# Kernel optimization log

Measured on AMD Instinct MI355X. Metric: run time of the kernel, lower is better.

## Reference

```python
import jax, jax.numpy as jnp
import numpy as np

EMBED_DIM = 1024
NUM_HEADS = 16
N_POS = 2048
BATCH = 4


def setup_inputs() -> dict:
    key = jax.random.key(0)
    k_x, k_w1, k_b1, k_wo, k_bo = jax.random.split(key, 5)
    s1 = 1.0 / np.sqrt(EMBED_DIM)
    x = jax.random.normal(k_x, (BATCH, N_POS, EMBED_DIM), dtype=jnp.float32)
    # torch Linear weights stored as [in, out] for x @ W + b
    W_qkv = jax.random.uniform(k_w1, (EMBED_DIM, 3 * EMBED_DIM), dtype=jnp.float32, minval=-s1, maxval=s1)
    b_qkv = jax.random.uniform(k_b1, (3 * EMBED_DIM,), dtype=jnp.float32, minval=-s1, maxval=s1)
    W_o = jax.random.uniform(k_wo, (EMBED_DIM, EMBED_DIM), dtype=jnp.float32, minval=-s1, maxval=s1)
    b_o = jax.random.uniform(k_bo, (EMBED_DIM,), dtype=jnp.float32, minval=-s1, maxval=s1)
    return {"x": x, "W_qkv": W_qkv, "b_qkv": b_qkv, "W_o": W_o, "b_o": b_o}


def reference(x, W_qkv, b_qkv, W_o, b_o):
    B, N, C = x.shape
    H = NUM_HEADS
    d_k = C // H
    qkv = x @ W_qkv + b_qkv                       # [B, N, 3C]
    q, k, v = jnp.split(qkv, 3, axis=-1)
    q = q.reshape(B, N, H, d_k).transpose(0, 2, 1, 3)  # [B, H, N, d_k]
    k = k.reshape(B, N, H, d_k).transpose(0, 2, 1, 3)
    v = v.reshape(B, N, H, d_k).transpose(0, 2, 1, 3)
    scores = jnp.einsum('bhqd,bhkd->bhqk', q, k) * (1.0 / np.sqrt(d_k))
    causal = jnp.tril(jnp.ones((N, N), dtype=bool))
    scores = jnp.where(causal, scores, -jnp.inf)
    attn = jax.nn.softmax(scores, axis=-1)
    out = jnp.einsum('bhqk,bhkd->bhqd', attn, v)  # [B, H, N, d_k]
    out = out.transpose(0, 2, 1, 3).reshape(B, N, C)
    return out @ W_o + b_o
```

## Files before the change

### kernel.cpp

```cpp
#include <hip/hip_runtime.h>
#include <hip/hip_bf16.h>

typedef __attribute__((ext_vector_type(8))) __bf16 bf16x8;
typedef __attribute__((ext_vector_type(4))) float f32x4;
typedef __attribute__((ext_vector_type(16))) float f32x16;
typedef __attribute__((ext_vector_type(4))) unsigned short u16x4;
typedef __attribute__((ext_vector_type(8))) unsigned short u16x8;
typedef __attribute__((ext_vector_type(4))) unsigned int u32x4;
typedef unsigned short u16;

#define MFMA16 __builtin_amdgcn_mfma_f32_16x16x32_bf16
#define MFMA32 __builtin_amdgcn_mfma_f32_32x32x16_bf16

#if __has_builtin(__builtin_amdgcn_exp2f)
#define EXP2F __builtin_amdgcn_exp2f
#else
#define EXP2F(x) __expf((x) * 0.69314718056f)
#endif

__device__ inline u16 f32_to_bf16_bits(float f) {
    unsigned u = __builtin_bit_cast(unsigned, f);
    unsigned r = u + 0x7FFFu + ((u >> 16) & 1u);
    return (u16)(r >> 16);
}

__device__ inline void g2l16(const void* g, void* l) {
    __builtin_amdgcn_global_load_lds(
        (const __attribute__((address_space(1))) unsigned int*)g,
        (__attribute__((address_space(3))) unsigned int*)l,
        16, 0, 0);
}

__device__ inline float red32_max(float x) { return fmaxf(x, __shfl_xor(x, 32)); }
__device__ inline float red32_sum(float x) { return x + __shfl_xor(x, 32); }

__global__ void cvt_bf16_kernel(const float* __restrict__ in, u16* __restrict__ out, int n) {
    int i = (blockIdx.x * 256 + threadIdx.x) * 4;
    if (i >= n) return;
    f32x4 v = *(const f32x4*)&in[i];
    u16x4 r;
#pragma unroll
    for (int j = 0; j < 4; ++j) r[j] = f32_to_bf16_bits(v[j]);
    *(u16x4*)&out[i] = r;
}

__global__ __launch_bounds__(256) void cvt_t_kernel(const float* __restrict__ W,
                                                    u16* __restrict__ WT, int K, int N) {
    const int w = threadIdx.x >> 6, l = threadIdx.x & 63;
    const int n = blockIdx.x * 64 + l;
    const int k0 = blockIdx.y * 32 + w * 8;
    u16x8 r;
#pragma unroll
    for (int i = 0; i < 8; ++i)
        r[i] = f32_to_bf16_bits(W[(size_t)(k0 + i) * N + n]);
    *(u16x8*)&WT[(size_t)n * K + k0] = r;
}

template <int STORE_BF16>
__global__ __launch_bounds__(256) void gemm_nt(
    const u16* __restrict__ A, const u16* __restrict__ BT,
    const float* __restrict__ bias, void* __restrict__ Cv,
    int M, int N, int K, int qcols, float qscale, int nbx)
{
    __shared__ __align__(16) u16 SM[24576];
    const int tid = threadIdx.x;
    const int w = tid >> 6, l = tid & 63;
    const int lr = l & 15, lh = l >> 4;
    const int wr = (w >> 1) * 64, wc = (w & 1) * 64;

    const int nwg = gridDim.x;
    const int swz = (blockIdx.x & 7) * (nwg >> 3) + (blockIdx.x >> 3);
    const int m0 = (swz / nbx) * 128;
    const int n0 = (swz % nbx) * 128;

    const int NT = K >> 5;

    const int f0 = tid, f1 = 256 + tid;
    const int r0 = f0 >> 2, r1 = f1 >> 2;
    const int cs0 = ((f0 & 3) ^ ((r0 >> 1) & 3)) * 8;
    const int cs1 = ((f1 & 3) ^ ((r1 >> 1) & 3)) * 8;
    const size_t arow0 = (size_t)(m0 + r0) * K, arow1 = (size_t)(m0 + r1) * K;
    const size_t brow0 = (size_t)(n0 + r0) * K, brow1 = (size_t)(n0 + r1) * K;

#define STAGE_TILE(t, set)                                                     \
    do {                                                                       \
        const int kk_ = (t) * 32;                                              \
        u16* dst_ = SM + (set) * 8192 + w * 512;                               \
        g2l16(A + arow0 + kk_ + cs0, dst_);                                    \
        g2l16(BT + brow0 + kk_ + cs0, dst_ + 4096);                            \
        g2l16(A + arow1 + kk_ + cs1, dst_ + 2048);                             \
        g2l16(BT + brow1 + kk_ + cs1, dst_ + 4096 + 2048);                     \
    } while (0)

    f32x4 acc[4][4];
#pragma unroll
    for (int m = 0; m < 4; ++m)
#pragma unroll
        for (int n = 0; n < 4; ++n) acc[m][n] = (f32x4)(0.0f);

    STAGE_TILE(0, 0);
    STAGE_TILE(1, 1);
    asm volatile("s_waitcnt vmcnt(4) lgkmcnt(0)\n\ts_barrier" ::: "memory");

    const int csw = (lr >> 1) & 3;
    int s0 = 0, s2 = 2;
    for (int t = 0; t < NT; ++t) {
        if (t + 2 < NT) STAGE_TILE(t + 2, s2);

        const u16* As = SM + s0 * 8192;
        const u16* Bs = As + 4096;
        bf16x8 af[4], bfr[4];
#pragma unroll
        for (int m = 0; m < 4; ++m)
            af[m] = *(const bf16x8*)&As[(wr + m * 16 + lr) * 32 + ((lh ^ csw) << 3)];
#pragma unroll
        for (int n = 0; n < 4; ++n)
            bfr[n] = *(const bf16x8*)&Bs[(wc + n * 16 + lr) * 32 + ((lh ^ csw) << 3)];
        __builtin_amdgcn_s_setprio(1);
#pragma unroll
        for (int m = 0; m < 4; ++m)
#pragma unroll
            for (int n = 0; n < 4; ++n)
                acc[m][n] = MFMA16(af[m], bfr[n], acc[m][n], 0, 0, 0);
        __builtin_amdgcn_s_setprio(0);

        if (t + 2 < NT)
            asm volatile("s_waitcnt vmcnt(4) lgkmcnt(0)\n\ts_barrier" ::: "memory");
        else if (t + 1 < NT)
            asm volatile("s_waitcnt vmcnt(0) lgkmcnt(0)\n\ts_barrier" ::: "memory");

        s0 = (s0 == 2) ? 0 : s0 + 1;
        s2 = (s2 == 2) ? 0 : s2 + 1;
    }
#undef STAGE_TILE

#pragma unroll
    for (int m = 0; m < 4; ++m) {
        int row = m0 + wr + m * 16 + lh * 4;
#pragma unroll
        for (int n = 0; n < 4; ++n) {
            int col = n0 + wc + n * 16 + lr;
            float bs = bias[col];
            float sc = (col < qcols) ? qscale : 1.0f;
#pragma unroll
            for (int j = 0; j < 4; ++j) {
                float v = (acc[m][n][j] + bs) * sc;
                if (STORE_BF16)
                    ((u16*)Cv)[(size_t)(row + j) * N + col] = f32_to_bf16_bits(v);
                else
                    ((float*)Cv)[(size_t)(row + j) * N + col] = v;
            }
        }
    }
}

__global__ __launch_bounds__(512, 1) void attn_kernel(
    const u16* __restrict__ qkv, u16* __restrict__ ctx)
{
    __shared__ __align__(16) u16 SM[32768];

    const int bid = blockIdx.x;
    const int xcd = bid & 7, jj = bid >> 3;
    const int bh = xcd * 8 + (jj >> 2);
    const int pr = jj & 3;
    const int b = bh >> 4, h = bh & 15;
    const size_t rowbase = (size_t)b * 2048;
    const int tid = threadIdx.x, w = tid >> 6, l = tid & 63;
    const int lq = l & 31, lk = l >> 5;

    const int rsub = l >> 3;
    const int cstage = l & 7;
    const int kchunk = cstage ^ rsub;

    bf16x8 vreg[2];

#pragma unroll
    for (int pass = 0; pass < 2; ++pass) {
        const int qt = pass ? (7 - pr) : pr;
        const int q0 = qt * 256;
        const int nt = 2 * qt + 2;
        const int qbase = q0 + w * 32;

        const u16* qp = qkv + (rowbase + qbase + lq) * 3072 + h * 64 + lk * 8;
        bf16x8 qf[4];
#pragma unroll
        for (int j = 0; j < 4; ++j) qf[j] = *(const bf16x8*)(qp + j * 16);

        f32x16 ot[2];
#pragma unroll
        for (int dt = 0; dt < 2; ++dt) ot[dt] = (f32x16)(0.0f);
        float m_run = -3e38f, l_run = 0.0f;

        __syncthreads();
#pragma unroll
        for (int p = 0; p < 2; ++p) {
            const int r = w * 16 + p * 8 + rsub;
            g2l16(qkv + (rowbase + r) * 3072 + 1024 + h * 64 + kchunk * 8,
                  SM + w * 1024 + p * 512);
            vreg[p] = *(const bf16x8*)(qkv + (rowbase + r) * 3072 + 2048 + h * 64 + cstage * 8);
        }
        asm volatile("s_waitcnt vmcnt(0)" ::: "memory");
#pragma unroll
        for (int p = 0; p < 2; ++p) {
            const int r = w * 16 + p * 8 + rsub;
#pragma unroll
            for (int i = 0; i < 8; ++i) {
                const int d = cstage * 8 + i;
                SM[16384 + ((d * 128 + r) ^ (((i ^ cstage) & 7) << 3))] = ((const u16*)&vreg[p])[i];
            }
        }
        __syncthreads();

        for (int t = 0; t < nt; ++t) {
            const int c = t & 1;
            const int kb = t * 128;
            u16* const Kb = SM + (c ? 8192 : 0);
            u16* const Vb = SM + 16384 + (c ? 8192 : 0);

            if (t + 1 < nt) {
                const int kb2 = kb + 128;
#pragma unroll
                for (int p = 0; p < 2; ++p) {
                    const int r = w * 16 + p * 8 + rsub;
                    g2l16(qkv + (rowbase + kb2 + r) * 3072 + 1024 + h * 64 + kchunk * 8,
                          SM + (c ? 0 : 8192) + w * 1024 + p * 512);
                    vreg[p] = *(const bf16x8*)(qkv + (rowbase + kb2 + r) * 3072 + 2048 + h * 64 + cstage * 8);
                }
            }

            if (kb <= qbase + 31) {
                bf16x8 kf[4][4];
#pragma unroll
                for (int kt = 0; kt < 4; ++kt)
#pragma unroll
                    for (int j = 0; j < 4; ++j)
                        kf[kt][j] = *(const bf16x8*)&Kb[((kt * 32 + lq) * 64 + j * 16 + lk * 8) ^ ((lq & 7) << 3)];

                f32x16 sf[4];
                __builtin_amdgcn_s_setprio(1);
#pragma unroll
                for (int kt = 0; kt < 4; ++kt) {
                    f32x16 z = (f32x16)(0.0f);
#pragma unroll
                    for (int j = 0; j < 4; ++j) z = MFMA32(kf[kt][j], qf[j], z, 0, 0, 0);
                    sf[kt] = z;
                }
                __builtin_amdgcn_s_setprio(0);

                float mt = -3e38f;
                if (kb + 127 > qbase) {
                    const int qrow = qbase + lq;
#pragma unroll
                    for (int kt = 0; kt < 4; ++kt)
#pragma unroll
                        for (int r = 0; r < 16; ++r) {
                            const int key = kb + kt * 32 + (r & 3) + 8 * (r >> 2) + 4 * lk;
                            float v = sf[kt][r];
                            if (key > qrow) v = -3e38f;
                            sf[kt][r] = v;
                            mt = fmaxf(mt, v);
                        }
                } else {
#pragma unroll
                    for (int kt = 0; kt < 4; ++kt)
#pragma unroll
                        for (int r = 0; r < 16; ++r) mt = fmaxf(mt, sf[kt][r]);
                }
                mt = red32_max(mt);

                const bool defer = __all(mt <= m_run + 16.0f);
                float mn = m_run;
                if (!defer) {
                    mn = fmaxf(m_run, mt);
                    const float alpha = EXP2F(m_run - mn);
                    m_run = mn;
                    l_run *= alpha;
#pragma unroll
                    for (int dt = 0; dt < 2; ++dt)
#pragma unroll
                        for (int r = 0; r < 16; ++r) ot[dt][r] *= alpha;
                }
                float rs = 0.0f;
#pragma unroll
                for (int kt = 0; kt < 4; ++kt)
#pragma unroll
                    for (int r = 0; r < 16; ++r) {
                        const float pp = EXP2F(sf[kt][r] - mn);
                        sf[kt][r] = pp;
                        rs += pp;
                    }
                l_run += red32_sum(rs);

                unsigned pc[4][4][2];
#pragma unroll
                for (int kt = 0; kt < 4; ++kt)
#pragma unroll
                    for (int rg = 0; rg < 4; ++rg) {
                        unsigned d0, d1;
                        asm("v_cvt_pk_bf16_f32 %0, %1, %2"
                            : "=v"(d0) : "v"((float)sf[kt][rg * 4 + 0]), "v"((float)sf[kt][rg * 4 + 1]));
                        asm("v_cvt_pk_bf16_f32 %0, %1, %2"
                            : "=v"(d1) : "v"((float)sf[kt][rg * 4 + 2]), "v"((float)sf[kt][rg * 4 + 3]));
                        pc[kt][rg][0] = d0;
                        pc[kt][rg][1] = d1;
                    }

                __builtin_amdgcn_s_setprio(1);
#pragma unroll
                for (int kt = 0; kt < 4; ++kt)
#pragma unroll
                    for (int hh = 0; hh < 2; ++hh) {
                        unsigned a0 = pc[kt][2 * hh][0], a1 = pc[kt][2 * hh][1];
                        unsigned b0 = pc[kt][2 * hh + 1][0], b1 = pc[kt][2 * hh + 1][1];
                        asm("v_permlane32_swap_b32 %0, %1" : "+v"(a0), "+v"(b0));
                        asm("v_permlane32_swap_b32 %0, %1" : "+v"(a1), "+v"(b1));
                        u32x4 wv = {a0, a1, b0, b1};
                        const bf16x8 pb = __builtin_bit_cast(bf16x8, wv);
                        const int k0 = 2 * kt + hh;
#pragma unroll
                        for (int dt = 0; dt < 2; ++dt) {
                            const int d = dt * 32 + lq;
                            const int vswz = ((d & 7) ^ (d >> 3)) & 7;
                            const bf16x8 vf = *(const bf16x8*)&Vb[((d * 128) + (k0 * 16 + lk * 8)) ^ (vswz << 3)];
                            ot[dt] = MFMA32(vf, pb, ot[dt], 0, 0, 0);
                        }
                    }
                __builtin_amdgcn_s_setprio(0);
            }

            asm volatile("s_waitcnt vmcnt(0)" ::: "memory");
            if (t + 1 < nt) {
                u16* const Vn = SM + 16384 + (c ? 0 : 8192);
#pragma unroll
                for (int p = 0; p < 2; ++p) {
                    const int r = w * 16 + p * 8 + rsub;
#pragma unroll
                    for (int i = 0; i < 8; ++i) {
                        const int d = cstage * 8 + i;
                        Vn[((d * 128 + r) ^ (((i ^ cstage) & 7) << 3))] = ((const u16*)&vreg[p])[i];
                    }
                }
            }
            __syncthreads();
        }

        u16* const out_l = SM + w * 2176;
        const float inv = 1.0f / l_run;
#pragma unroll
        for (int dt = 0; dt < 2; ++dt)
#pragma unroll
            for (int r = 0; r < 16; ++r) {
                const int d = dt * 32 + (r & 3) + 8 * (r >> 2) + 4 * lk;
                out_l[lq * 68 + d] = f32_to_bf16_bits(ot[dt][r] * inv);
            }
#pragma unroll
        for (int rr = 0; rr < 4; ++rr) {
            const int row = rr * 8 + (l >> 3);
            const bf16x8 v = *(const bf16x8*)&out_l[row * 68 + (l & 7) * 8];
            *(bf16x8*)(ctx + (rowbase + qbase + row) * 1024 + h * 64 + (l & 7) * 8) = v;
        }
    }
}

extern "C" void kernel_launch(void* const* d_in, const int* in_sizes, int n_in,
                              void* d_out, int out_size, void* d_ws, size_t ws_size,
                              hipStream_t stream) {
    const float* x      = (const float*)d_in[0];
    const float* W_qkv  = (const float*)d_in[1];
    const float* b_qkv  = (const float*)d_in[2];
    const float* W_o    = (const float*)d_in[3];
    const float* b_o    = (const float*)d_in[4];
    float* out = (float*)d_out;

    const int M = 4 * 2048;
    const int C = 1024;
    u16* qkv   = (u16*)d_ws;
    u16* xb    = qkv   + (size_t)M * 3 * C;
    u16* wqkvt = xb    + (size_t)M * C;
    u16* ctx   = wqkvt + (size_t)3 * C * C;
    u16* wot   = ctx   + (size_t)M * C;

    const float SCQ = 0.125f * 1.44269504089f;

    cvt_bf16_kernel<<<(M * C) / (256 * 4), 256, 0, stream>>>(x, xb, M * C);
    cvt_t_kernel<<<dim3(3 * C / 64, C / 32), 256, 0, stream>>>(W_qkv, wqkvt, C, 3 * C);
    cvt_t_kernel<<<dim3(C / 64, C / 32), 256, 0, stream>>>(W_o, wot, C, C);

    gemm_nt<1><<<(3 * C / 128) * (M / 128), 256, 0, stream>>>(xb, wqkvt, b_qkv, qkv,
                                                              M, 3 * C, C, C, SCQ, 3 * C / 128);

    attn_kernel<<<256, 512, 0, stream>>>(qkv, ctx);

    gemm_nt<0><<<(C / 128) * (M / 128), 256, 0, stream>>>(ctx, wot, b_o, out,
                                                          M, C, C, 0, 1.0f, C / 128);
}
```

Baseline: 167.0 us.

## Use 256x128 tile GEMM with triple-buffered LDS for QKV projection

Adds a new GEMM kernel for the QKV projection that computes 256x128 output tiles per workgroup, with each wave owning a 128x64 block. K-slices are held in a three-stage LDS ring buffer, and loads for step t+2 are issued while step t is being multiplied. The larger tile raises arithmetic intensity and the deeper pipeline is meant to hide global-load latency. The cost is more LDS and accumulator registers per workgroup, which may lower occupancy, and the grid is halved to 768 workgroups.

```diff
diff --git a/kernel.cpp b/kernel.cpp
--- a/kernel.cpp
+++ b/kernel.cpp
@@ -54,6 +54,109 @@
     for (int i = 0; i < 8; ++i)
         r[i] = f32_to_bf16_bits(W[(size_t)(k0 + i) * N + n]);
     *(u16x8*)&WT[(size_t)n * K + k0] = r;
+}
+
+template <int STORE_BF16>
+__global__ __launch_bounds__(256) void gemm_nt5(
+    const u16* __restrict__ A, const u16* __restrict__ BT,
+    const float* __restrict__ bias, void* __restrict__ Cv,
+    int M, int N, int K, int qcols, float qscale, int nbx)
+{
+    __shared__ __align__(16) u16 SM[36864];
+    const int tid = threadIdx.x;
+    const int w = tid >> 6, l = tid & 63;
+    const int lr = l & 15, lh = l >> 4;
+    const int wr = (w >> 1) * 128;
+    const int wc = (w & 1) * 64;
+
+    const int nwg = gridDim.x;
+    const int swz = (blockIdx.x & 7) * (nwg >> 3) + (blockIdx.x >> 3);
+    const int m0 = (swz / nbx) * 256;
+    const int n0 = (swz % nbx) * 128;
+
+    const int NT = K >> 5;
+
+    const int rr = tid >> 2;
+    const int cs = ((tid & 3) ^ ((tid >> 3) & 3)) * 8;
+    size_t aoff[4], boff[2];
+#pragma unroll
+    for (int p = 0; p < 4; ++p) aoff[p] = (size_t)(m0 + p * 64 + rr) * K + cs;
+#pragma unroll
+    for (int p = 0; p < 2; ++p) boff[p] = (size_t)(n0 + p * 64 + rr) * K + cs;
+    u16* const wbase = SM + (size_t)(tid >> 6) * 512;
+
+#define STAGE5(t, set)                                                         \
+    do {                                                                       \
+        const int kk_ = (t) * 32;                                              \
+        u16* d_ = wbase + (set) * 12288;                                       \
+        g2l16(A + aoff[0] + kk_, d_);                                          \
+        g2l16(A + aoff[1] + kk_, d_ + 2048);                                   \
+        g2l16(A + aoff[2] + kk_, d_ + 4096);                                   \
+        g2l16(A + aoff[3] + kk_, d_ + 6144);                                   \
+        g2l16(BT + boff[0] + kk_, d_ + 8192);                                  \
+        g2l16(BT + boff[1] + kk_, d_ + 10240);                                 \
+    } while (0)
+
+    f32x4 acc[8][4];
+#pragma unroll
+    for (int m = 0; m < 8; ++m)
+#pragma unroll
+        for (int n = 0; n < 4; ++n) acc[m][n] = (f32x4)(0.0f);
+
+    STAGE5(0, 0);
+    STAGE5(1, 1);
+    asm volatile("s_waitcnt vmcnt(6) lgkmcnt(0)\n\ts_barrier" ::: "memory");
+
+    const int csw = (lr >> 1) & 3;
+    int s0 = 0, s2 = 2;
+    for (int t = 0; t < NT; ++t) {
+        if (t + 2 < NT) STAGE5(t + 2, s2);
+
+        const u16* As = SM + s0 * 12288;
+        const u16* Bs = As + 8192;
+        bf16x8 af[8], bfr[4];
+#pragma unroll
+        for (int m = 0; m < 8; ++m)
+            af[m] = *(const bf16x8*)&As[(wr + m * 16 + lr) * 32 + ((lh ^ csw) << 3)];
+#pragma unroll
+        for (int n = 0; n < 4; ++n)
+            bfr[n] = *(const bf16x8*)&Bs[(wc + n * 16 + lr) * 32 + ((lh ^ csw) << 3)];
+        __builtin_amdgcn_s_setprio(1);
+#pragma unroll
+        for (int m = 0; m < 8; ++m)
+#pragma unroll
+            for (int n = 0; n < 4; ++n)
+                acc[m][n] = MFMA16(af[m], bfr[n], acc[m][n], 0, 0, 0);
+        __builtin_amdgcn_s_setprio(0);
+
+        if (t + 2 < NT)
+            asm volatile("s_waitcnt vmcnt(6) lgkmcnt(0)\n\ts_barrier" ::: "memory");
+        else if (t + 1 < NT)
+            asm volatile("s_waitcnt vmcnt(0) lgkmcnt(0)\n\ts_barrier" ::: "memory");
+
+        s0 = (s0 == 2) ? 0 : s0 + 1;
+        s2 = (s2 == 2) ? 0 : s2 + 1;
+    }
+#undef STAGE5
+
+#pragma unroll
+    for (int m = 0; m < 8; ++m) {
+        int row = m0 + wr + m * 16 + lh * 4;
+#pragma unroll
+        for (int n = 0; n < 4; ++n) {
+            int col = n0 + wc + n * 16 + lr;
+            float bs = bias[col];
+            float sc = (col < qcols) ? qscale : 1.0f;
+#pragma unroll
+            for (int j = 0; j < 4; ++j) {
+                float v = (acc[m][n][j] + bs) * sc;
+                if (STORE_BF16)
+                    ((u16*)Cv)[(size_t)(row + j) * N + col] = f32_to_bf16_bits(v);
+                else
+                    ((float*)Cv)[(size_t)(row + j) * N + col] = v;
+            }
+        }
+    }
 }
 
 template <int STORE_BF16>
@@ -386,8 +489,8 @@
     cvt_t_kernel<<<dim3(3 * C / 64, C / 32), 256, 0, stream>>>(W_qkv, wqkvt, C, 3 * C);
     cvt_t_kernel<<<dim3(C / 64, C / 32), 256, 0, stream>>>(W_o, wot, C, C);
 
-    gemm_nt<1><<<(3 * C / 128) * (M / 128), 256, 0, stream>>>(xb, wqkvt, b_qkv, qkv,
-                                                              M, 3 * C, C, C, SCQ, 3 * C / 128);
+    gemm_nt5<1><<<(M / 256) * (3 * C / 128), 256, 0, stream>>>(xb, wqkvt, b_qkv, qkv,
+                                                               M, 3 * C, C, C, SCQ, 3 * C / 128);
 
     attn_kernel<<<256, 512, 0, stream>>>(qkv, ctx);
 
```

Result: slower. 180.2 us (+7.9%).

## Use 256x256 eight-wave GEMM with staggered prefetch for QKV projection

Applied to the files above, without the earlier changes.

Adds a new GEMM kernel with 512 threads and 256x256 output tiles, double-buffered 128KB LDS, and next-tile loads split into four quarter stages interleaved with MFMA phases. The kernel raises MFMA priority during compute and replaces the 128x128 kernel for the QKV projection. The aim is more data reuse per LDS load and better overlap of global loads with compute. In exchange, the larger tile yields only 384 workgroups at one per CU and adds extra barriers, which could hurt latency hiding.

```diff
diff --git a/kernel.cpp b/kernel.cpp
--- a/kernel.cpp
+++ b/kernel.cpp
@@ -54,6 +54,121 @@
     for (int i = 0; i < 8; ++i)
         r[i] = f32_to_bf16_bits(W[(size_t)(k0 + i) * N + n]);
     *(u16x8*)&WT[(size_t)n * K + k0] = r;
+}
+
+template <int STORE_BF16>
+__global__ __launch_bounds__(512) void gemm_8p(
+    const u16* __restrict__ A, const u16* __restrict__ BT,
+    const float* __restrict__ bias, void* __restrict__ Cv,
+    int M, int N, int K, int qcols, float qscale, int nbx)
+{
+    __shared__ __align__(16) u16 SM[65536];
+    const int tid = threadIdx.x;
+    const int w = tid >> 6, l = tid & 63;
+    const int lr = l & 15, lh = l >> 4;
+    const int wr = (w >> 2) * 128;
+    const int wc = (w & 3) * 64;
+
+    const int nwg = gridDim.x;
+    const int swz = (blockIdx.x & 7) * (nwg >> 3) + (blockIdx.x >> 3);
+    const int m0 = (swz / nbx) * 256;
+    const int n0 = (swz % nbx) * 256;
+
+    const int NT = K >> 6;
+
+    const int f0 = tid, f1 = 512 + tid;
+    const int r0 = f0 >> 3, r1 = f1 >> 3;
+    const int c0 = ((f0 & 7) ^ (r0 & 7)) * 8;
+    const int c1 = ((f1 & 7) ^ (r1 & 7)) * 8;
+
+#define STAGE_HALF(j, h)                                                        \
+    do {                                                                        \
+        const int kk_ = (j) * 64;                                               \
+        u16* db_ = SM + (((j) & 1) << 15) + (h) * 8192;                         \
+        const u16* src_ = ((h) < 2) ? (A + (size_t)(m0 + (h) * 128) * K)        \
+                                    : (BT + (size_t)(n0 + ((h) - 2) * 128) * K);\
+        g2l16(src_ + (size_t)r0 * K + kk_ + c0, db_ + f0 * 8);                  \
+        g2l16(src_ + (size_t)r1 * K + kk_ + c1, db_ + f1 * 8);                  \
+    } while (0)
+
+    f32x4 acc[8][4];
+#pragma unroll
+    for (int m = 0; m < 8; ++m)
+#pragma unroll
+        for (int n = 0; n < 4; ++n) acc[m][n] = (f32x4)(0.0f);
+
+    STAGE_HALF(0, 0); STAGE_HALF(0, 1); STAGE_HALF(0, 2); STAGE_HALF(0, 3);
+
+    const int swk = lr & 7;
+    for (int j = 0; j < NT; ++j) {
+        const u16* Abuf = SM + ((j & 1) << 15);
+        const u16* Bbuf = Abuf + 16384;
+
+#pragma unroll
+        for (int q = 0; q < 4; ++q) {
+            const int mq = q & 1, nq = q >> 1;
+
+            if (q == 0) {
+                if (j + 1 < NT) {
+                    STAGE_HALF(j + 1, 0);
+                    asm volatile("s_waitcnt vmcnt(2)\n\ts_barrier" ::: "memory");
+                } else {
+                    asm volatile("s_waitcnt vmcnt(0)\n\ts_barrier" ::: "memory");
+                }
+            }
+
+            bf16x8 af[4][2], bfr[2][2];
+#pragma unroll
+            for (int m = 0; m < 4; ++m) {
+                const int row = wr + mq * 64 + m * 16 + lr;
+#pragma unroll
+                for (int ks = 0; ks < 2; ++ks)
+                    af[m][ks] = *(const bf16x8*)&Abuf[row * 64 + ((ks * 4 + lh) ^ swk) * 8];
+            }
+#pragma unroll
+            for (int n = 0; n < 2; ++n) {
+                const int row = wc + nq * 32 + n * 16 + lr;
+#pragma unroll
+                for (int ks = 0; ks < 2; ++ks)
+                    bfr[n][ks] = *(const bf16x8*)&Bbuf[row * 64 + ((ks * 4 + lh) ^ swk) * 8];
+            }
+
+            if (q != 0 && j + 1 < NT) STAGE_HALF(j + 1, q);
+
+            asm volatile("s_barrier\n\ts_waitcnt lgkmcnt(0)" ::: "memory");
+            __builtin_amdgcn_s_setprio(1);
+#pragma unroll
+            for (int m = 0; m < 4; ++m)
+#pragma unroll
+                for (int n = 0; n < 2; ++n)
+#pragma unroll
+                    for (int ks = 0; ks < 2; ++ks)
+                        acc[mq * 4 + m][nq * 2 + n] =
+                            MFMA16(af[m][ks], bfr[n][ks], acc[mq * 4 + m][nq * 2 + n], 0, 0, 0);
+            __builtin_amdgcn_s_setprio(0);
+            asm volatile("s_barrier" ::: "memory");
+        }
+    }
+#undef STAGE_HALF
+
+#pragma unroll
+    for (int m = 0; m < 8; ++m) {
+        int row = m0 + wr + m * 16 + lh * 4;
+#pragma unroll
+        for (int n = 0; n < 4; ++n) {
+            int col = n0 + wc + n * 16 + lr;
+            float bs = bias[col];
+            float sc = (col < qcols) ? qscale : 1.0f;
+#pragma unroll
+            for (int j = 0; j < 4; ++j) {
+                float v = (acc[m][n][j] + bs) * sc;
+                if (STORE_BF16)
+                    ((u16*)Cv)[(size_t)(row + j) * N + col] = f32_to_bf16_bits(v);
+                else
+                    ((float*)Cv)[(size_t)(row + j) * N + col] = v;
+            }
+        }
+    }
 }
 
 template <int STORE_BF16>
@@ -386,8 +501,8 @@
     cvt_t_kernel<<<dim3(3 * C / 64, C / 32), 256, 0, stream>>>(W_qkv, wqkvt, C, 3 * C);
     cvt_t_kernel<<<dim3(C / 64, C / 32), 256, 0, stream>>>(W_o, wot, C, C);
 
-    gemm_nt<1><<<(3 * C / 128) * (M / 128), 256, 0, stream>>>(xb, wqkvt, b_qkv, qkv,
-                                                              M, 3 * C, C, C, SCQ, 3 * C / 128);
+    gemm_8p<1><<<(M / 256) * (3 * C / 256), 512, 0, stream>>>(xb, wqkvt, b_qkv, qkv,
+                                                              M, 3 * C, C, C, SCQ, 3 * C / 256);
 
     attn_kernel<<<256, 512, 0, stream>>>(qkv, ctx);
 
```

Result: slower. 177.0 us (+5.9%).
